# Kernel tuning notes

Hardware: AMD Instinct MI355X
Metric: run time of the kernel (lower is better)

## Reference

```python
import jax, jax.numpy as jnp
import numpy as np

EPS = 1e-6
SCALE = 1.0
GRID_HEIGHT = 4.0
GRID_RES_Y = 1.0


def _perspective(mat, vec):
    # mat [3,4], vec [...,3] -> (points [...,2], flag [...,3])
    homog = jnp.einsum('ij,...j->...i', mat[:, :3], vec) + mat[:, 3]
    pos = homog[..., 2:3] > 0
    flag = jnp.concatenate([pos, pos, jnp.ones_like(pos)], axis=-1).astype(homog.dtype)
    homog = homog * flag  # zero x,y behind camera; z kept (flag[...,-1]=True)
    return homog[..., :2] / homog[..., 2:3], flag


def _fisheye(pts, k, D, flag):
    cx, cy, fx, fy = k[0, 2], k[1, 2], k[0, 0], k[1, 1]
    x = (pts[..., 0] - cx) / fx
    y = (pts[..., 1] - cy) / fy
    r = jnp.sqrt(x * x + y * y)
    th = jnp.arctan(r)
    t2 = th * th
    rad = th * (1 + D[0] * t2 + D[1] * t2 ** 2 + D[2] * t2 ** 3 + D[5] * t2 ** 4) / r
    xd = x * rad * fx + cx
    yd = y * rad * fy + cy
    return jnp.stack([xd, yd], axis=-1) * flag[..., :2]


def _pinhole(pts, k, D, flag):
    cx, cy, fx, fy = k[0, 2], k[1, 2], k[0, 0], k[1, 1]
    x = (pts[..., 0] - cx) / fx
    y = (pts[..., 1] - cy) / fy
    k1, k2, k3, p1, p2 = D[0], D[1], D[2], D[3], D[4]
    r2 = x * x + y * y
    poly = 1 + k1 * r2 + k2 * r2 * r2 + k3 * r2 * r2 * r2
    xd = x * poly + (2 * p1 * x * y + p2 * (r2 + 2 * x * x))
    yd = y * poly + (p1 * (r2 + 2 * y * y) + 2 * p2 * x * y)
    return jnp.stack([xd * fx + cx, yd * fy + cy], axis=-1) * flag[..., :2]


def _bilinear(img, coords):
    # torch F.grid_sample(align_corners=True, padding_mode='border'); img [C,H,W], coords [...,2] in [-1,1]
    C, H, W = img.shape
    x = jnp.clip((coords[..., 0] + 1) * 0.5 * (W - 1), 0.0, W - 1)
    y = jnp.clip((coords[..., 1] + 1) * 0.5 * (H - 1), 0.0, H - 1)
    x0 = jnp.floor(x)
    y0 = jnp.floor(y)
    wx = x - x0
    wy = y - y0
    x0i = x0.astype(jnp.int32)
    y0i = y0.astype(jnp.int32)
    x1i = jnp.minimum(x0i + 1, W - 1)
    y1i = jnp.minimum(y0i + 1, H - 1)
    flat = img.reshape(C, H * W)

    def g(yi, xi):
        return jnp.take(flat, (yi * W + xi).reshape(-1), axis=1).reshape((C,) + coords.shape[:-1])

    v00 = g(y0i, x0i)
    v01 = g(y0i, x1i)
    v10 = g(y1i, x0i)
    v11 = g(y1i, x1i)
    return v00 * (1 - wx) * (1 - wy) + v01 * wx * (1 - wy) + v10 * (1 - wx) * wy + v11 * wx * wy


def _per_image(feature, k, imu2c, post_rot, post_tran, undist, corner):
    C, Hf, Wf = feature.shape
    calib = k @ imu2c                                  # [3,4]
    pts, flag = _perspective(calib, corner)            # pts [Ny,Zd,Xd,2]
    pts = jnp.where(undist[-1] == 1,
                    _fisheye(pts, k, undist, flag),
                    _pinhole(pts, k, undist, flag))
    pts = jnp.einsum('ij,...j->...i', post_rot[:2, :2], pts) + post_tran[:2]
    nc = jnp.clip(2.0 * (pts / SCALE) - 1.0, -1.0, 1.0)  # [Ny,Zd,Xd,2]
    s0, s1 = slice(None, -1), slice(1, None)
    # 8 voxel corners -> [8, Ny-1, D, Wd, 2]
    corners8 = jnp.stack([nc[a, b, c] for a in (s0, s1) for b in (s0, s1) for c in (s0, s1)], axis=0)
    left = corners8[..., 0].min(0)
    right = corners8[..., 0].max(0)
    top = corners8[..., 1].min(0)
    bot = corners8[..., 1].max(0)
    Nh, D, Wd = left.shape
    bbox = jnp.stack([left, top, right, bot], axis=-1).reshape(Nh, D * Wd, 4)
    area = (bbox[..., 2] - bbox[..., 0]) * (bbox[..., 3] - bbox[..., 1]) * Hf * Wf * 0.25 + EPS  # [Nh,P]
    integ = jnp.cumsum(jnp.cumsum(feature, axis=-1), axis=-2)  # integral image [C,Hf,Wf]
    tl = _bilinear(integ, bbox[..., 0:2])
    br = _bilinear(integ, bbox[..., 2:4])
    tr = _bilinear(integ, jnp.stack([bbox[..., 2], bbox[..., 1]], axis=-1))
    bl = _bilinear(integ, jnp.stack([bbox[..., 0], bbox[..., 3]], axis=-1))
    vox = (tl + br - tr - bl) / area * (area > EPS)    # [C,Nh,P]
    return vox.reshape(C * Nh, D, Wd)                  # neck == '2d'


def _forward(features, ks, imu2cs, post_rots, post_trans, undists, grid):
    ys = -jnp.arange(0.0, GRID_HEIGHT, GRID_RES_Y) + GRID_HEIGHT / 2.0
    y_corners = jnp.stack([jnp.zeros_like(ys), ys, jnp.zeros_like(ys)], axis=-1)  # [Ny,3]
    corners = grid[:, None] + y_corners[None, :, None, None, :]                   # [B,Ny,Zd,Xd,3]
    per_cam = jax.vmap(_per_image, in_axes=(0, 0, 0, 0, 0, 0, None))

    def per_batch(f, k, m, pr, pt, ud, c):
        # drop_idx = [] -> all cameras kept; max over cameras
        return per_cam(f, k, m, pr, pt, ud, c).max(axis=0)

    return jax.vmap(per_batch)(features, ks, imu2cs, post_rots, post_trans, undists, corners)


def setup_inputs():
    key = jax.random.key(0)
    B, N, C, Hf, Wf = 1, 6, 64, 64, 176
    Zd = Xd = 129
    kf, ku = jax.random.split(key, 2)
    features = jax.random.normal(kf, (B, N, C, Hf, Wf), jnp.float32)
    # intrinsics (realistic pinhole values keep the projection numerically sane)
    K = np.zeros((B, N, 3, 3), np.float32)
    K[..., 0, 0] = 600.0
    K[..., 1, 1] = 600.0
    K[..., 0, 2] = 704.0
    K[..., 1, 2] = 256.0
    K[..., 2, 2] = 1.0
    ks = jnp.asarray(K)
    # extrinsics: per-camera yaw + small translation
    m = np.zeros((B, N, 3, 4), np.float32)
    for i in range(N):
        th = 0.25 * (i - 2.5)
        R = np.array([[np.cos(th), 0.0, np.sin(th)],
                      [0.0, 1.0, 0.0],
                      [-np.sin(th), 0.0, np.cos(th)]], np.float32)
        m[:, i, :, :3] = R
        m[:, i, :, 3] = np.array([0.1 * i, -1.5, 0.2], np.float32)
    imu2cs = jnp.asarray(m)
    pr = np.zeros((B, N, 3, 3), np.float32)
    pr[..., 0, 0] = 1.0 / 1408.0
    pr[..., 1, 1] = 1.0 / 512.0
    pr[..., 2, 2] = 1.0
    post_rots = jnp.asarray(pr)
    post_trans = jnp.zeros((B, N, 3), jnp.float32)
    und = 0.01 * np.array(jax.random.normal(ku, (B, N, 7)), np.float32)
    und[..., 6] = 0.0
    und[:, :3, 6] = 1.0  # first 3 cameras fisheye, rest pinhole
    undists = jnp.asarray(und)
    x = np.linspace(-40.0, 40.0, Xd, dtype=np.float32)
    z = np.linspace(3.0, 80.0, Zd, dtype=np.float32)
    zz, xx = np.meshgrid(z, x, indexing='ij')
    g = np.stack([xx, np.zeros_like(xx), zz], axis=-1)[None]  # [1,Zd,Xd,3]
    grid = jnp.asarray(np.broadcast_to(g, (B, Zd, Xd, 3)).copy())
    return {"features": features, "ks": ks, "imu2cs": imu2cs, "post_rots": post_rots,
            "post_trans": post_trans, "undists": undists, "grid": grid}


def reference(features, ks, imu2cs, post_rots, post_trans, undists, grid):
    return _forward(features, ks, imu2cs, post_rots, post_trans, undists, grid)
```

## Files before the change

### kernel.cpp

```cpp
#include <hip/hip_runtime.h>
#include <math.h>

#define NCAM 6
#define C_CH 64
#define HF   64
#define WF   176
#define GDIM 129
#define NY   4
#define NH   3
#define DD   128
#define WDIM 128
#define NP   (DD*WDIM)

#define ROWB (WF*C_CH*4)
#define COLB (C_CH*4)
#define IMGB ((size_t)HF*WF*C_CH*4)


__device__ __forceinline__ float bcf(int x) {
    return __builtin_bit_cast(float, x);
}

__global__ __launch_bounds__(256) void k_rowcum(const float* __restrict__ feat,
                                                float* __restrict__ rowsum)
{
    __shared__ float T[WF * 65];
    __shared__ float S[4][C_CH];
    __shared__ float OFF[4][C_CH];
    const int h   = blockIdx.x;
    const int n   = blockIdx.y;
    const int tid = threadIdx.x;

    for (int idx = tid; idx < C_CH * WF; idx += 256) {
        const int cc = idx / WF;
        const int w  = idx % WF;
        T[w*65 + cc] = feat[((size_t)(n*C_CH + cc)*HF + h)*WF + w];
    }
    __syncthreads();
    {
        const int cc = tid & 63, seg = tid >> 6;
        const int w0 = seg * 44;
        float run = 0.0f;
        #pragma unroll
        for (int i = 0; i < 44; ++i) {
            run += T[(w0 + i)*65 + cc];
            T[(w0 + i)*65 + cc] = run;
        }
        S[seg][cc] = run;
    }
    __syncthreads();
    {
        const int cc = tid & 63, seg = tid >> 6;
        float off = 0.0f;
        #pragma unroll
        for (int s = 0; s < 3; ++s)
            if (s < seg) off += S[s][cc];
        OFF[seg][cc] = off;
    }
    __syncthreads();
    float* outp = rowsum + (size_t)(n*HF + h) * (WF * C_CH);
    for (int idx = tid; idx < WF * C_CH; idx += 256) {
        const int w  = idx >> 6;
        const int cc = idx & 63;
        outp[idx] = T[w*65 + cc] + OFF[w/44][cc];
    }
}

__global__ __launch_bounds__(256) void k_colcum(float* __restrict__ integ)
{
    __shared__ float tA[4][C_CH];
    const int x  = blockIdx.x;
    const int n  = blockIdx.y;
    const int c  = threadIdx.x & 63;
    const int hq = threadIdx.x >> 6;

    float* base = integ + (size_t)n*HF*WF*C_CH + (size_t)x * C_CH + c;
    float e[16];
    #pragma unroll
    for (int i = 0; i < 16; ++i)
        e[i] = base[(size_t)(hq*16 + i) * (WF*C_CH)];
    #pragma unroll
    for (int i = 1; i < 16; ++i)
        e[i] += e[i-1];
    tA[hq][c] = e[15];
    __syncthreads();
    float off = 0.0f;
    #pragma unroll
    for (int s = 0; s < 3; ++s)
        if (s < hq) off += tA[s][c];
    #pragma unroll
    for (int i = 0; i < 16; ++i)
        base[(size_t)(hq*16 + i) * (WF*C_CH)] = e[i] + off;
}

__global__ void k_boxproj(const float* __restrict__ ks,
                          const float* __restrict__ imu2cs,
                          const float* __restrict__ post_rots,
                          const float* __restrict__ post_trans,
                          const float* __restrict__ undists,
                          const float* __restrict__ grid,
                          int4* __restrict__ bp)
{
    const int idx = blockIdx.x * blockDim.x + threadIdx.x;
    if (idx >= NCAM * NH * NP) return;
    const int vox = idx / NCAM;
    const int n   = idx - vox * NCAM;
    const int nh  = vox / NP;
    const int p   = vox - nh * NP;
    const int d   = p / WDIM;
    const int wd  = p - d * WDIM;

    const float* k  = ks         + n * 9;
    const float* m  = imu2cs     + n * 12;
    const float* pr = post_rots  + n * 9;
    const float* pt = post_trans + n * 3;
    const float* D  = undists    + n * 7;

    float cal[12];
    #pragma unroll
    for (int i = 0; i < 3; ++i)
        #pragma unroll
        for (int j = 0; j < 4; ++j)
            cal[i*4+j] = k[i*3+0]*m[0*4+j] + k[i*3+1]*m[1*4+j] + k[i*3+2]*m[2*4+j];

    const float fx = k[0], fy = k[4], cx = k[2], cy = k[5];
    const float rfx = 1.0f / fx, rfy = 1.0f / fy;
    const bool fish = (D[6] == 1.0f);
    const float D0 = D[0], D1 = D[1], D2 = D[2], D3 = D[3], D4 = D[4], D5 = D[5];

    float left = 1e30f, right = -1e30f, top = 1e30f, bot = -1e30f;
    #pragma unroll
    for (int a = 0; a < 2; ++a) {
        const float vy = 2.0f - (float)(nh + a);
        #pragma unroll
        for (int b = 0; b < 2; ++b) {
            #pragma unroll
            for (int cc = 0; cc < 2; ++cc) {
                const int gz = d + b, gx = wd + cc;
                const float vx = grid[(gz*GDIM + gx)*3 + 0];
                const float vz = grid[(gz*GDIM + gx)*3 + 2];

                const float hx = cal[0]*vx + cal[1]*vy + cal[2]*vz  + cal[3];
                const float hy = cal[4]*vx + cal[5]*vy + cal[6]*vz  + cal[7];
                const float hz = cal[8]*vx + cal[9]*vy + cal[10]*vz + cal[11];

                const float fl = (hz > 0.0f) ? 1.0f : 0.0f;
                const float rhz = __builtin_amdgcn_rcpf(hz);
                const float px = (hx * fl) * rhz;
                const float py = (hy * fl) * rhz;

                const float x = (px - cx) * rfx;
                const float y = (py - cy) * rfy;

                float xd, yd;
                if (fish) {
                    const float rr = sqrtf(x*x + y*y);
                    const float th = atanf(rr);
                    const float t2 = th * th;
                    const float t4 = t2 * t2;
                    const float rad = th * (1.0f + D0*t2 + D1*t4 + D2*(t2*t4) + D5*(t4*t4))
                                      * __builtin_amdgcn_rcpf(rr);
                    xd = x * rad * fx + cx;
                    yd = y * rad * fy + cy;
                } else {
                    const float r2 = x*x + y*y;
                    const float poly = 1.0f + D0*r2 + D1*r2*r2 + D2*r2*r2*r2;
                    const float xdd = x*poly + (2.0f*D3*x*y + D4*(r2 + 2.0f*x*x));
                    const float ydd = y*poly + (D3*(r2 + 2.0f*y*y) + 2.0f*D4*x*y);
                    xd = xdd * fx + cx;
                    yd = ydd * fy + cy;
                }
                xd *= fl; yd *= fl;

                const float qx = pr[0]*xd + pr[1]*yd + pt[0];
                const float qy = pr[3]*xd + pr[4]*yd + pt[1];
                const float ncx = fminf(fmaxf(2.0f*qx - 1.0f, -1.0f), 1.0f);
                const float ncy = fminf(fmaxf(2.0f*qy - 1.0f, -1.0f), 1.0f);

                left  = fminf(left,  ncx);  right = fmaxf(right, ncx);
                top   = fminf(top,   ncy);  bot   = fmaxf(bot,   ncy);
            }
        }
    }

    const float area = (right - left) * (bot - top) * (float)HF * (float)WF * 0.25f + 1e-6f;

    const float xLp = fminf(fmaxf((left  + 1.0f) * 0.5f * (float)(WF-1), 0.0f), (float)(WF-1));
    const float xRp = fminf(fmaxf((right + 1.0f) * 0.5f * (float)(WF-1), 0.0f), (float)(WF-1));
    const float yTp = fminf(fmaxf((top   + 1.0f) * 0.5f * (float)(HF-1), 0.0f), (float)(HF-1));
    const float yBp = fminf(fmaxf((bot   + 1.0f) * 0.5f * (float)(HF-1), 0.0f), (float)(HF-1));
    const float xL0 = floorf(xLp), xR0 = floorf(xRp), yT0 = floorf(yTp), yB0 = floorf(yBp);

    const int pyx = (int)yT0 | ((int)yB0 << 8) | ((int)xL0 << 16) | ((int)xR0 << 24);

    int4 o0, o1;
    o0.x = pyx;
    o0.y = __builtin_bit_cast(int, xLp - xL0);
    o0.z = __builtin_bit_cast(int, xRp - xR0);
    o0.w = __builtin_bit_cast(int, yTp - yT0);
    o1.x = __builtin_bit_cast(int, yBp - yB0);
    o1.y = __builtin_bit_cast(int, area);
    o1.z = 0; o1.w = 0;
    bp[(size_t)idx*2 + 0] = o0;
    bp[(size_t)idx*2 + 1] = o1;
}

__global__ __launch_bounds__(256, 6) void k_sample(const float* __restrict__ integ,
                                                   const int* __restrict__ bpi,
                                                   float* __restrict__ out)
{
    __shared__ float sm[32][65];
    const int bx   = blockIdx.x;
    const int xcd  = bx & 7;
    const int slot = bx >> 3;
    const int gt   = xcd * 192 + slot;
    const int nh   = gt >> 9;
    const int p0   = (gt & 511) * 32;
    const int tid  = threadIdx.x;
    const int wave = __builtin_amdgcn_readfirstlane(tid >> 6);
    const int c    = tid & 63;
    const int pl   = (c < 48) ? c : (c - 48);

    const int* bpw = bpi + (size_t)(nh*NP + p0 + wave*8) * 48;

    int vpc = bpw[pl];
    #pragma unroll 1
    for (int j = 0; j < 8; ++j) {
        int vpn = vpc;
        if (j < 7) vpn = bpw[(j + 1) * 48 + pl];

        float vmax = -3.402823466e38f;
        #pragma unroll
        for (int pr2 = 0; pr2 < 3; ++pr2) {
            const int camA = pr2*2, camB = pr2*2 + 1;
            const int fA = __builtin_amdgcn_readlane(vpc, camA*8 + 0);
            const float wxlA = bcf(__builtin_amdgcn_readlane(vpc, camA*8 + 1));
            const float wxrA = bcf(__builtin_amdgcn_readlane(vpc, camA*8 + 2));
            const float wytA = bcf(__builtin_amdgcn_readlane(vpc, camA*8 + 3));
            const float wybA = bcf(__builtin_amdgcn_readlane(vpc, camA*8 + 4));
            const float arA  = bcf(__builtin_amdgcn_readlane(vpc, camA*8 + 5));
            const int fB = __builtin_amdgcn_readlane(vpc, camB*8 + 0);
            const float wxlB = bcf(__builtin_amdgcn_readlane(vpc, camB*8 + 1));
            const float wxrB = bcf(__builtin_amdgcn_readlane(vpc, camB*8 + 2));
            const float wytB = bcf(__builtin_amdgcn_readlane(vpc, camB*8 + 3));
            const float wybB = bcf(__builtin_amdgcn_readlane(vpc, camB*8 + 4));
            const float arB  = bcf(__builtin_amdgcn_readlane(vpc, camB*8 + 5));

            float tA[16], tB[16];
            {
                const int yT = fA & 255, yB2 = (fA >> 8) & 255;
                const int xL = (fA >> 16) & 255, xR = (fA >> 24) & 255;
                const int r0 = yT * ROWB, r2 = yB2 * ROWB;
                const int c0 = xL * COLB, c2 = xR * COLB;
                const char* b = (const char*)integ + (size_t)camA * IMGB;
                #pragma unroll
                for (int rr = 0; rr < 4; ++rr) {
                    const int ro = ((rr < 2) ? r0 : r2) + ((rr & 1) ? ROWB : 0);
                    #pragma unroll
                    for (int cc2 = 0; cc2 < 4; ++cc2) {
                        const int co = ((cc2 < 2) ? c0 : c2) + ((cc2 & 1) ? COLB : 0);
                        tA[rr*4 + cc2] = ((const float*)(b + (size_t)(ro + co)))[c];
                    }
                }
            }
            {
                const int yT = fB & 255, yB2 = (fB >> 8) & 255;
                const int xL = (fB >> 16) & 255, xR = (fB >> 24) & 255;
                const int r0 = yT * ROWB, r2 = yB2 * ROWB;
                const int c0 = xL * COLB, c2 = xR * COLB;
                const char* b = (const char*)integ + (size_t)camB * IMGB;
                #pragma unroll
                for (int rr = 0; rr < 4; ++rr) {
                    const int ro = ((rr < 2) ? r0 : r2) + ((rr & 1) ? ROWB : 0);
                    #pragma unroll
                    for (int cc2 = 0; cc2 < 4; ++cc2) {
                        const int co = ((cc2 < 2) ? c0 : c2) + ((cc2 & 1) ? COLB : 0);
                        tB[rr*4 + cc2] = ((const float*)(b + (size_t)(ro + co)))[c];
                    }
                }
            }

            {
                const float A0 = fmaf(wxlA, tA[1]  - tA[0],  tA[0]);
                const float B0 = fmaf(wxrA, tA[3]  - tA[2],  tA[2]);
                const float A1 = fmaf(wxlA, tA[5]  - tA[4],  tA[4]);
                const float B1 = fmaf(wxrA, tA[7]  - tA[6],  tA[6]);
                const float A2 = fmaf(wxlA, tA[9]  - tA[8],  tA[8]);
                const float B2 = fmaf(wxrA, tA[11] - tA[10], tA[10]);
                const float A3 = fmaf(wxlA, tA[13] - tA[12], tA[12]);
                const float B3 = fmaf(wxrA, tA[15] - tA[14], tA[14]);
                const float d0 = A0 - B0, d1 = A1 - B1;
                const float e0 = B2 - A2, e1 = B3 - A3;
                const float s = fmaf(wytA, d1 - d0, d0) + fmaf(wybA, e1 - e0, e0);
                float v = s * __builtin_amdgcn_rcpf(arA);
                v = (arA > 1e-6f) ? v : 0.0f;
                vmax = fmaxf(vmax, v);
            }
            {
                const float A0 = fmaf(wxlB, tB[1]  - tB[0],  tB[0]);
                const float B0 = fmaf(wxrB, tB[3]  - tB[2],  tB[2]);
                const float A1 = fmaf(wxlB, tB[5]  - tB[4],  tB[4]);
                const float B1 = fmaf(wxrB, tB[7]  - tB[6],  tB[6]);
                const float A2 = fmaf(wxlB, tB[9]  - tB[8],  tB[8]);
                const float B2 = fmaf(wxrB, tB[11] - tB[10], tB[10]);
                const float A3 = fmaf(wxlB, tB[13] - tB[12], tB[12]);
                const float B3 = fmaf(wxrB, tB[15] - tB[14], tB[14]);
                const float d0 = A0 - B0, d1 = A1 - B1;
                const float e0 = B2 - A2, e1 = B3 - A3;
                const float s = fmaf(wytB, d1 - d0, d0) + fmaf(wybB, e1 - e0, e0);
                float v = s * __builtin_amdgcn_rcpf(arB);
                v = (arB > 1e-6f) ? v : 0.0f;
                vmax = fmaxf(vmax, v);
            }
        }
        sm[wave*8 + j][c] = vmax;
        vpc = vpn;
    }
    __syncthreads();
    #pragma unroll
    for (int it = 0; it < 8; ++it) {
        const int idx = it*256 + tid;
        const int jj = idx & 31;
        const int cc = idx >> 5;
        out[(size_t)(cc*NH + nh)*NP + p0 + jj] = sm[jj][cc];
    }
}

extern "C" void kernel_launch(void* const* d_in, const int* in_sizes, int n_in,
                              void* d_out, int out_size, void* d_ws, size_t ws_size,
                              hipStream_t stream)
{
    const float* feats      = (const float*)d_in[0];
    const float* ks         = (const float*)d_in[1];
    const float* imu2cs     = (const float*)d_in[2];
    const float* post_rots  = (const float*)d_in[3];
    const float* post_trans = (const float*)d_in[4];
    const float* undists    = (const float*)d_in[5];
    const float* grid       = (const float*)d_in[6];
    float* out = (float*)d_out;

    char* ws = (char*)d_ws;
    size_t off = 0;
    float* integ = (float*)(ws + off);
    off += (size_t)NCAM * IMGB + 65536;
    off = (off + 255) & ~(size_t)255;
    int4* bp = (int4*)(ws + off);
    off += (size_t)NCAM * NH * NP * 32 + 256;
    (void)ws_size; (void)in_sizes; (void)n_in; (void)out_size;

    dim3 g1(HF, NCAM);
    k_rowcum<<<g1, 256, 0, stream>>>(feats, integ);

    dim3 g2(WF, NCAM);
    k_colcum<<<g2, 256, 0, stream>>>(integ);

    dim3 g3((NCAM*NH*NP + 255)/256);
    k_boxproj<<<g3, 256, 0, stream>>>(ks, imu2cs, post_rots, post_trans, undists, grid, bp);

    dim3 g4(NP/32 * NH);
    k_sample<<<g4, 256, 0, stream>>>(integ, (const int*)bp, out);
}
```

Before: 148.6 us.

## Store integral image as x-adjacent float2 pairs to halve sampling gathers

The column-cumsum kernel now writes an interleaved buffer in which each entry holds the integral value at x and at x+1 as a float2. The sampling kernel then fetches each horizontal neighbour pair with a single 8-byte load, so it issues 8 loads per camera instead of 16. The cost is a second buffer twice the size of the integral image plus an extra read pass in the cumsum kernel, and the sampler touches twice as many bytes per load.

New measurement: 176.8 us. 19.0% more time.

```diff
diff --git a/kernel.cpp b/kernel.cpp
--- a/kernel.cpp
+++ b/kernel.cpp
@@ -12,9 +12,9 @@
 #define WDIM 128
 #define NP   (DD*WDIM)
 
-#define ROWB (WF*C_CH*4)
-#define COLB (C_CH*4)
-#define IMGB ((size_t)HF*WF*C_CH*4)
+#define PROWB (WF*C_CH*8)
+#define PCOLB (C_CH*8)
+#define PIMGB ((size_t)HF*WF*C_CH*8)
 
 
 __device__ __forceinline__ float bcf(int x) {
@@ -66,31 +66,43 @@
     }
 }
 
-__global__ __launch_bounds__(256) void k_colcum(float* __restrict__ integ)
-{
-    __shared__ float tA[4][C_CH];
+__global__ __launch_bounds__(256) void k_paircol(const float* __restrict__ rowsum,
+                                                 float2* __restrict__ pbuf)
+{
+    __shared__ float tA[4][C_CH], tB[4][C_CH];
     const int x  = blockIdx.x;
     const int n  = blockIdx.y;
+    const int x1 = min(x + 1, WF - 1);
     const int c  = threadIdx.x & 63;
     const int hq = threadIdx.x >> 6;
 
-    float* base = integ + (size_t)n*HF*WF*C_CH + (size_t)x * C_CH + c;
-    float e[16];
-    #pragma unroll
-    for (int i = 0; i < 16; ++i)
-        e[i] = base[(size_t)(hq*16 + i) * (WF*C_CH)];
-    #pragma unroll
-    for (int i = 1; i < 16; ++i)
-        e[i] += e[i-1];
-    tA[hq][c] = e[15];
-    __syncthreads();
-    float off = 0.0f;
+    const float* base0 = rowsum + (size_t)n*HF*WF*C_CH + (size_t)x  * C_CH + c;
+    const float* base1 = rowsum + (size_t)n*HF*WF*C_CH + (size_t)x1 * C_CH + c;
+    float eA[16], eB[16];
+    #pragma unroll
+    for (int i = 0; i < 16; ++i) {
+        const int h = hq*16 + i;
+        eA[i] = base0[(size_t)h * (WF*C_CH)];
+        eB[i] = base1[(size_t)h * (WF*C_CH)];
+    }
+    #pragma unroll
+    for (int i = 1; i < 16; ++i) {
+        eA[i] += eA[i-1];
+        eB[i] += eB[i-1];
+    }
+    tA[hq][c] = eA[15];
+    tB[hq][c] = eB[15];
+    __syncthreads();
+    float offA = 0.0f, offB = 0.0f;
     #pragma unroll
     for (int s = 0; s < 3; ++s)
-        if (s < hq) off += tA[s][c];
-    #pragma unroll
-    for (int i = 0; i < 16; ++i)
-        base[(size_t)(hq*16 + i) * (WF*C_CH)] = e[i] + off;
+        if (s < hq) { offA += tA[s][c]; offB += tB[s][c]; }
+    float2* outp = pbuf + ((size_t)n*HF*WF + x) * C_CH + c;
+    #pragma unroll
+    for (int i = 0; i < 16; ++i) {
+        const int h = hq*16 + i;
+        outp[(size_t)h * (WF*C_CH)] = make_float2(eA[i] + offA, eB[i] + offB);
+    }
 }
 
 __global__ void k_boxproj(const float* __restrict__ ks,
@@ -205,7 +217,7 @@
     bp[(size_t)idx*2 + 1] = o1;
 }
 
-__global__ __launch_bounds__(256, 6) void k_sample(const float* __restrict__ integ,
+__global__ __launch_bounds__(256, 6) void k_sample(const float2* __restrict__ pbuf,
                                                    const int* __restrict__ bpi,
                                                    float* __restrict__ out)
 {
@@ -246,49 +258,47 @@
             const float wybB = bcf(__builtin_amdgcn_readlane(vpc, camB*8 + 4));
             const float arB  = bcf(__builtin_amdgcn_readlane(vpc, camB*8 + 5));
 
-            float tA[16], tB[16];
+            float2 tA[8], tB[8];
             {
                 const int yT = fA & 255, yB2 = (fA >> 8) & 255;
                 const int xL = (fA >> 16) & 255, xR = (fA >> 24) & 255;
-                const int r0 = yT * ROWB, r2 = yB2 * ROWB;
-                const int c0 = xL * COLB, c2 = xR * COLB;
-                const char* b = (const char*)integ + (size_t)camA * IMGB;
-                #pragma unroll
-                for (int rr = 0; rr < 4; ++rr) {
-                    const int ro = ((rr < 2) ? r0 : r2) + ((rr & 1) ? ROWB : 0);
-                    #pragma unroll
-                    for (int cc2 = 0; cc2 < 4; ++cc2) {
-                        const int co = ((cc2 < 2) ? c0 : c2) + ((cc2 & 1) ? COLB : 0);
-                        tA[rr*4 + cc2] = ((const float*)(b + (size_t)(ro + co)))[c];
-                    }
-                }
+                const int r0 = yT * PROWB, r2 = yB2 * PROWB;
+                const int cl = xL * PCOLB, cr = xR * PCOLB;
+                const char* b = (const char*)pbuf + (size_t)camA * PIMGB + (size_t)c * 8;
+                tA[0] = *(const float2*)(b + (size_t)(r0 + cl));
+                tA[1] = *(const float2*)(b + (size_t)(r0 + cr));
+                tA[2] = *(const float2*)(b + (size_t)(r0 + PROWB + cl));
+                tA[3] = *(const float2*)(b + (size_t)(r0 + PROWB + cr));
+                tA[4] = *(const float2*)(b + (size_t)(r2 + cl));
+                tA[5] = *(const float2*)(b + (size_t)(r2 + cr));
+                tA[6] = *(const float2*)(b + (size_t)(r2 + PROWB + cl));
+                tA[7] = *(const float2*)(b + (size_t)(r2 + PROWB + cr));
             }
             {
                 const int yT = fB & 255, yB2 = (fB >> 8) & 255;
                 const int xL = (fB >> 16) & 255, xR = (fB >> 24) & 255;
-                const int r0 = yT * ROWB, r2 = yB2 * ROWB;
-                const int c0 = xL * COLB, c2 = xR * COLB;
-                const char* b = (const char*)integ + (size_t)camB * IMGB;
-                #pragma unroll
-                for (int rr = 0; rr < 4; ++rr) {
-                    const int ro = ((rr < 2) ? r0 : r2) + ((rr & 1) ? ROWB : 0);
-                    #pragma unroll
-                    for (int cc2 = 0; cc2 < 4; ++cc2) {
-                        const int co = ((cc2 < 2) ? c0 : c2) + ((cc2 & 1) ? COLB : 0);
-                        tB[rr*4 + cc2] = ((const float*)(b + (size_t)(ro + co)))[c];
-                    }
-                }
+                const int r0 = yT * PROWB, r2 = yB2 * PROWB;
+                const int cl = xL * PCOLB, cr = xR * PCOLB;
+                const char* b = (const char*)pbuf + (size_t)camB * PIMGB + (size_t)c * 8;
+                tB[0] = *(const float2*)(b + (size_t)(r0 + cl));
+                tB[1] = *(const float2*)(b + (size_t)(r0 + cr));
+                tB[2] = *(const float2*)(b + (size_t)(r0 + PROWB + cl));
+                tB[3] = *(const float2*)(b + (size_t)(r0 + PROWB + cr));
+                tB[4] = *(const float2*)(b + (size_t)(r2 + cl));
+                tB[5] = *(const float2*)(b + (size_t)(r2 + cr));
+                tB[6] = *(const float2*)(b + (size_t)(r2 + PROWB + cl));
+                tB[7] = *(const float2*)(b + (size_t)(r2 + PROWB + cr));
             }
 
             {
-                const float A0 = fmaf(wxlA, tA[1]  - tA[0],  tA[0]);
-                const float B0 = fmaf(wxrA, tA[3]  - tA[2],  tA[2]);
-                const float A1 = fmaf(wxlA, tA[5]  - tA[4],  tA[4]);
-                const float B1 = fmaf(wxrA, tA[7]  - tA[6],  tA[6]);
-                const float A2 = fmaf(wxlA, tA[9]  - tA[8],  tA[8]);
-                const float B2 = fmaf(wxrA, tA[11] - tA[10], tA[10]);
-                const float A3 = fmaf(wxlA, tA[13] - tA[12], tA[12]);
-                const float B3 = fmaf(wxrA, tA[15] - tA[14], tA[14]);
+                const float A0 = fmaf(wxlA, tA[0].y - tA[0].x, tA[0].x);
+                const float B0 = fmaf(wxrA, tA[1].y - tA[1].x, tA[1].x);
+                const float A1 = fmaf(wxlA, tA[2].y - tA[2].x, tA[2].x);
+                const float B1 = fmaf(wxrA, tA[3].y - tA[3].x, tA[3].x);
+                const float A2 = fmaf(wxlA, tA[4].y - tA[4].x, tA[4].x);
+                const float B2 = fmaf(wxrA, tA[5].y - tA[5].x, tA[5].x);
+                const float A3 = fmaf(wxlA, tA[6].y - tA[6].x, tA[6].x);
+                const float B3 = fmaf(wxrA, tA[7].y - tA[7].x, tA[7].x);
                 const float d0 = A0 - B0, d1 = A1 - B1;
                 const float e0 = B2 - A2, e1 = B3 - A3;
                 const float s = fmaf(wytA, d1 - d0, d0) + fmaf(wybA, e1 - e0, e0);
@@ -297,14 +307,14 @@
                 vmax = fmaxf(vmax, v);
             }
             {
-                const float A0 = fmaf(wxlB, tB[1]  - tB[0],  tB[0]);
-                const float B0 = fmaf(wxrB, tB[3]  - tB[2],  tB[2]);
-                const float A1 = fmaf(wxlB, tB[5]  - tB[4],  tB[4]);
-                const float B1 = fmaf(wxrB, tB[7]  - tB[6],  tB[6]);
-                const float A2 = fmaf(wxlB, tB[9]  - tB[8],  tB[8]);
-                const float B2 = fmaf(wxrB, tB[11] - tB[10], tB[10]);
-                const float A3 = fmaf(wxlB, tB[13] - tB[12], tB[12]);
-                const float B3 = fmaf(wxrB, tB[15] - tB[14], tB[14]);
+                const float A0 = fmaf(wxlB, tB[0].y - tB[0].x, tB[0].x);
+                const float B0 = fmaf(wxrB, tB[1].y - tB[1].x, tB[1].x);
+                const float A1 = fmaf(wxlB, tB[2].y - tB[2].x, tB[2].x);
+                const float B1 = fmaf(wxrB, tB[3].y - tB[3].x, tB[3].x);
+                const float A2 = fmaf(wxlB, tB[4].y - tB[4].x, tB[4].x);
+                const float B2 = fmaf(wxrB, tB[5].y - tB[5].x, tB[5].x);
+                const float A3 = fmaf(wxlB, tB[6].y - tB[6].x, tB[6].x);
+                const float B3 = fmaf(wxrB, tB[7].y - tB[7].x, tB[7].x);
                 const float d0 = A0 - B0, d1 = A1 - B1;
                 const float e0 = B2 - A2, e1 = B3 - A3;
                 const float s = fmaf(wytB, d1 - d0, d0) + fmaf(wybB, e1 - e0, e0);
@@ -341,22 +351,25 @@
 
     char* ws = (char*)d_ws;
     size_t off = 0;
-    float* integ = (float*)(ws + off);
-    off += (size_t)NCAM * IMGB + 65536;
+    float* rowsum = (float*)(ws + off);
+    off += (size_t)NCAM * HF * WF * C_CH * 4;
+    off = (off + 255) & ~(size_t)255;
+    float2* pbuf = (float2*)(ws + off);
+    off += (size_t)NCAM * PIMGB + PROWB;
     off = (off + 255) & ~(size_t)255;
     int4* bp = (int4*)(ws + off);
     off += (size_t)NCAM * NH * NP * 32 + 256;
     (void)ws_size; (void)in_sizes; (void)n_in; (void)out_size;
 
     dim3 g1(HF, NCAM);
-    k_rowcum<<<g1, 256, 0, stream>>>(feats, integ);
+    k_rowcum<<<g1, 256, 0, stream>>>(feats, rowsum);
 
     dim3 g2(WF, NCAM);
-    k_colcum<<<g2, 256, 0, stream>>>(integ);
+    k_paircol<<<g2, 256, 0, stream>>>(rowsum, pbuf);
 
     dim3 g3((NCAM*NH*NP + 255)/256);
     k_boxproj<<<g3, 256, 0, stream>>>(ks, imu2cs, post_rots, post_trans, undists, grid, bp);
 
     dim3 g4(NP/32 * NH);
-    k_sample<<<g4, 256, 0, stream>>>(integ, (const int*)bp, out);
-}
+    k_sample<<<g4, 256, 0, stream>>>(pbuf, (const int*)bp, out);
+}
```
